# Kernel tuning notes

Hardware: AMD Instinct MI355X
Metric: run time of the kernel (lower is better)

The kernel has to match this reference:

```python
import jax, jax.numpy as jnp
import numpy as np

A = 81          # agents / zones (9x9 grid)
DMAX = 5        # max neighborhood size (self + 4-neighbors)
NGLOB = 48      # global obs block width
HID = 128
B = 16384
LN_EPS = 1e-12  # tf.contrib.layers.layer_norm epsilon
BN_EPS = 1e-3   # tf.contrib.layers.batch_norm epsilon
NEG = -1e30


def _grid_adjacency():
    side = 9
    idx = np.zeros((A, DMAX), np.int32)
    mask = np.zeros((A, DMAX), bool)
    for i in range(A):
        r, c = divmod(i, side)
        nb = [i]
        for dr, dc in ((-1, 0), (1, 0), (0, -1), (0, 1)):
            rr, cc = r + dr, c + dc
            if 0 <= rr < side and 0 <= cc < side:
                nb.append(rr * side + cc)
        idx[i, :len(nb)] = nb
        mask[i, :len(nb)] = True
    return jnp.asarray(idx), jnp.asarray(mask)


def setup_inputs() -> dict:
    key = jax.random.key(0)
    ks = jax.random.split(key, 8)
    neigh_idx, neigh_mask = _grid_adjacency()
    in_dim = 2 * DMAX + NGLOB  # padded local obs width (58)
    s = 0.05
    return {
        "obs": jax.random.normal(ks[0], (B, 210), jnp.float32),
        "neigh_idx": neigh_idx,
        "neigh_mask": neigh_mask,
        "W1": jax.random.normal(ks[1], (A, in_dim, HID), jnp.float32) * s,
        "b1": jnp.zeros((A, HID), jnp.float32),
        "ln1_g": jnp.ones((A, HID), jnp.float32),
        "ln1_b": jnp.zeros((A, HID), jnp.float32),
        "bn1_b": jnp.zeros((A, HID), jnp.float32),
        "W2": jax.random.normal(ks[2], (A, HID, HID), jnp.float32) * s,
        "b2": jnp.zeros((A, HID), jnp.float32),
        "ln2_g": jnp.ones((A, HID), jnp.float32),
        "ln2_b": jnp.zeros((A, HID), jnp.float32),
        "bn2_b": jnp.zeros((A, HID), jnp.float32),
        "Wout": jax.random.normal(ks[3], (A, HID, DMAX), jnp.float32) * s,
        "bout": jnp.zeros((A, DMAX), jnp.float32),
    }


def _layer_norm(x, g, b):
    mu = jnp.mean(x, axis=-1, keepdims=True)
    var = jnp.mean(jnp.square(x - mu), axis=-1, keepdims=True)
    return (x - mu) * jax.lax.rsqrt(var + LN_EPS) * g[:, None, :] + b[:, None, :]


def _batch_norm(x, beta):
    # training-mode batch norm over the batch axis (axis=1), center only (scale=False)
    mu = jnp.mean(x, axis=1, keepdims=True)
    var = jnp.mean(jnp.square(x - mu), axis=1, keepdims=True)
    return (x - mu) * jax.lax.rsqrt(var + BN_EPS) + beta[:, None, :]


def reference(obs, neigh_idx, neigh_mask, W1, b1, ln1_g, ln1_b, bn1_b,
              W2, b2, ln2_g, ln2_b, bn2_b, Wout, bout):
    m = neigh_mask[:, None, :].astype(obs.dtype)          # [A,1,DMAX]
    g1 = obs[:, NGLOB + neigh_idx].transpose(1, 0, 2)      # [A,B,DMAX] zone block 1
    g2 = obs[:, NGLOB + 81 + neigh_idx].transpose(1, 0, 2)  # [A,B,DMAX] zone block 2
    glob = jnp.broadcast_to(obs[None, :, :NGLOB], (A, obs.shape[0], NGLOB))
    x = jnp.concatenate([g1 * m, g2 * m, glob], axis=-1)   # [A,B,58] (padded slots zeroed)

    h = jnp.einsum('abi,aio->abo', x, W1) + b1[:, None, :]
    h = jax.nn.relu(_batch_norm(_layer_norm(h, ln1_g, ln1_b), bn1_b))
    h = jnp.einsum('abi,aio->abo', h, W2) + b2[:, None, :]
    h = jax.nn.relu(_batch_norm(_layer_norm(h, ln2_g, ln2_b), bn2_b))

    logits = jnp.einsum('abi,aid->abd', h, Wout) + bout[:, None, :]  # [A,B,DMAX]
    logits = jnp.where(neigh_mask[:, None, :], logits, NEG)
    p = jax.nn.softmax(logits, axis=-1) * m                # masked softmax over valid neighbors

    oh = jax.nn.one_hot(neigh_idx, A, dtype=p.dtype)       # [A,DMAX,81] scatter map
    out = jnp.einsum('abd,adn->abn', p, oh)                # scatter into fixed 81-vector
    return out.transpose(1, 0, 2)                          # [B,A,81]
```

## Files before the change

### kernel.cpp

```cpp
#include <hip/hip_runtime.h>
#include <stdint.h>
#include <stddef.h>

#define N_AG 81

typedef __bf16 bf16x8 __attribute__((ext_vector_type(8)));
typedef float f32x4 __attribute__((ext_vector_type(4)));
typedef uint32_t u32v4 __attribute__((ext_vector_type(4)));
typedef uint32_t u32v2 __attribute__((ext_vector_type(2)));

#define PB 0
#define PG 128
#define PBT 256

#define SWZ(row, off) ((uint32_t)(off) ^ (((uint32_t)(row) & 7u) << 4))

__device__ __forceinline__ unsigned short b2u(__bf16 h) {
  return __builtin_bit_cast(unsigned short, h);
}

__device__ __forceinline__ f32x4 f4z() { f32x4 v; v[0]=0.f; v[1]=0.f; v[2]=0.f; v[3]=0.f; return v; }

__device__ __forceinline__ bf16x8 ld_frag(const uint8_t* p) {
  u32v4 v = *(const u32v4*)p;
  return __builtin_bit_cast(bf16x8, v);
}

__device__ __forceinline__ f32x4 mfma16(bf16x8 a, bf16x8 b, f32x4 c) {
  return __builtin_amdgcn_mfma_f32_16x16x32_bf16(a, b, c, 0, 0, 0);
}

__device__ __forceinline__ uint8_t* yslot(float* out, int b, int a) {
  size_t base = (size_t)b * 26244 + (size_t)a * 324;
  uint32_t pad = (uint32_t)(64 - (base & 63)) & 63u;
  return (uint8_t*)out + base + pad;
}

__device__ __forceinline__ float wave16_sum(float v) {
  v += __builtin_bit_cast(float, __builtin_amdgcn_update_dpp(0, __builtin_bit_cast(int, v), 0xB1, 0xF, 0xF, true));
  v += __builtin_bit_cast(float, __builtin_amdgcn_update_dpp(0, __builtin_bit_cast(int, v), 0x4E, 0xF, 0xF, true));
  v += __builtin_bit_cast(float, __builtin_amdgcn_update_dpp(0, __builtin_bit_cast(int, v), 0x141, 0xF, 0xF, true));
  v += __builtin_bit_cast(float, __builtin_amdgcn_update_dpp(0, __builtin_bit_cast(int, v), 0x140, 0xF, 0xF, true));
  return v;
}

__device__ __forceinline__ bf16x8 mk_frag(const unsigned short (&us)[8]) {
  u32v4 pk;
  pk[0] = (uint32_t)us[0] | ((uint32_t)us[1] << 16);
  pk[1] = (uint32_t)us[2] | ((uint32_t)us[3] << 16);
  pk[2] = (uint32_t)us[4] | ((uint32_t)us[5] << 16);
  pk[3] = (uint32_t)us[6] | ((uint32_t)us[7] << 16);
  return __builtin_bit_cast(bf16x8, pk);
}

__device__ __forceinline__ bf16x8 bn_frag(u32v4 yv, const f32x4 (&cf)[4]) {
  bf16x8 r;
  #pragma unroll
  for (int j = 0; j < 8; ++j) {
    uint32_t us = (j & 1) ? (yv[j >> 1] >> 16) : (yv[j >> 1] & 0xffffu);
    float f = __builtin_bit_cast(float, us << 16);
    float h = fmaf(f, cf[j >> 1][(j & 1) * 2], cf[j >> 1][(j & 1) * 2 + 1]);
    r[j] = (__bf16)fmaxf(h, 0.f);
  }
  return r;
}

__device__ __forceinline__ void bias_ln(f32x4 (&acc)[8][2], const float* s_par, int g) {
  #pragma unroll
  for (int nf = 0; nf < 2; ++nf) {
    float s = 0.f, qs = 0.f;
    #pragma unroll
    for (int mf = 0; mf < 8; ++mf) {
      #pragma unroll
      for (int rg = 0; rg < 4; ++rg) {
        float tv = acc[mf][nf][rg] + s_par[PB + 16 * mf + 4 * g + rg];
        acc[mf][nf][rg] = tv;
        s += tv;
        qs = fmaf(tv, tv, qs);
      }
    }
    s += __shfl_xor(s, 16);  s += __shfl_xor(s, 32);
    qs += __shfl_xor(qs, 16); qs += __shfl_xor(qs, 32);
    float mu = s * (1.f / 128.f);
    float var = qs * (1.f / 128.f) - mu * mu;
    float rstd = rsqrtf(var + 1e-12f);
    #pragma unroll
    for (int mf = 0; mf < 8; ++mf) {
      #pragma unroll
      for (int rg = 0; rg < 4; ++rg) {
        int o = 16 * mf + 4 * g + rg;
        acc[mf][nf][rg] = (acc[mf][nf][rg] - mu) * rstd * s_par[PG + o] + s_par[PBT + o];
      }
    }
  }
}

__device__ __forceinline__ void stats_lds(const f32x4 (&acc)[8][2],
                                          float (&s_red)[2][4][128],
                                          int wv, int g, int q) {
  #pragma unroll
  for (int mf = 0; mf < 8; ++mf) {
    #pragma unroll
    for (int rg = 0; rg < 4; ++rg) {
      float a0v = acc[mf][0][rg], a1v = acc[mf][1][rg];
      float s = a0v + a1v;
      float qq = fmaf(a0v, a0v, a1v * a1v);
      s = wave16_sum(s);
      qq = wave16_sum(qq);
      if (q == 0) {
        int o = 16 * mf + 4 * g + rg;
        s_red[0][wv][o] += s;
        s_red[1][wv][o] += qq;
      }
    }
  }
}

__device__ __forceinline__ void pack_lds(const f32x4 (&acc)[8][2], uint8_t* s_y,
                                         int wv, int g, int q) {
  #pragma unroll
  for (int nf = 0; nf < 2; ++nf) {
    uint32_t row = 32 * wv + 16 * nf + q;
    #pragma unroll
    for (int mf = 0; mf < 8; ++mf) {
      u32v2 pk;
      pk[0] = (uint32_t)b2u((__bf16)acc[mf][nf][0]) | ((uint32_t)b2u((__bf16)acc[mf][nf][1]) << 16);
      pk[1] = (uint32_t)b2u((__bf16)acc[mf][nf][2]) | ((uint32_t)b2u((__bf16)acc[mf][nf][3]) << 16);
      *(u32v2*)(s_y + row * 256 + SWZ(row, 32 * mf + 8 * g)) = pk;
    }
  }
}

__device__ __forceinline__ void burst_out(const uint8_t* s_y, float* out, int tile, int a, int t) {
  const int row = t >> 1, half = t & 1;
  uint8_t* sp = yslot(out, tile * 128 + row, a) + half * 128;
  #pragma unroll
  for (int j = 0; j < 8; ++j) {
    u32v4 v = *(const u32v4*)(s_y + row * 256 + SWZ(row, half * 128 + 16 * j));
    *(u32v4*)(sp + 16 * j) = v;
  }
}

__device__ __forceinline__ void load_yregs(u32v4 (&yr)[8], const float* out, int tile, int a, int t) {
  const int row = t >> 1, half = t & 1;
  const uint8_t* sp = yslot((float*)out, tile * 128 + row, a) + half * 128;
  #pragma unroll
  for (int j = 0; j < 8; ++j) yr[j] = *(const u32v4*)(sp + 16 * j);
}

__device__ __forceinline__ void write_yregs(uint8_t* s_y, const u32v4 (&yr)[8], int t) {
  const int row = t >> 1, half = t & 1;
  #pragma unroll
  for (int j = 0; j < 8; ++j)
    *(u32v4*)(s_y + row * 256 + SWZ(row, half * 128 + 16 * j)) = yr[j];
}

__global__ void prep_w1(const float* __restrict__ W1, uint8_t* __restrict__ w1img) {
  const int a = blockIdx.x, t = threadIdx.x;
  for (int i = t; i < 128 * 64; i += 256) {
    int o = i & 127, kk = i >> 7;
    float v;
    if (kk < 48)      v = W1[((size_t)a * 58 + (10 + kk)) * 128 + o];
    else if (kk < 58) v = W1[((size_t)a * 58 + (kk - 48)) * 128 + o];
    else              v = 0.f;
    uint32_t cb = 2u * kk;
    uint32_t phys = o * 128 + (((cb & ~15u) ^ (((uint32_t)o & 7u) << 4)) | (cb & 15u));
    *(unsigned short*)(w1img + (size_t)a * 16384 + phys) = b2u((__bf16)v);
  }
}

__global__ void prep_w2wo(const float* __restrict__ W2, const float* __restrict__ Wout,
                          uint8_t* __restrict__ w2img, uint8_t* __restrict__ woimg) {
  const int a = blockIdx.x, t = threadIdx.x;
  for (int i = t; i < 128 * 128; i += 256) {
    int o = i & 127, kk = i >> 7;
    float v = W2[((size_t)a * 128 + kk) * 128 + o];
    uint32_t cb = 2u * kk;
    uint32_t phys = o * 256 + (((cb & ~15u) ^ (((uint32_t)o & 7u) << 4)) | (cb & 15u));
    *(unsigned short*)(w2img + (size_t)a * 32768 + phys) = b2u((__bf16)v);
  }
  for (int i = t; i < 16 * 128; i += 256) {
    int k = i & 127, d = i >> 7;
    float v = (d < 5) ? Wout[((size_t)a * 128 + k) * 5 + d] : 0.f;
    uint32_t cb = 2u * k;
    uint32_t phys = d * 256 + (((cb & ~15u) ^ (((uint32_t)d & 7u) << 4)) | (cb & 15u));
    *(unsigned short*)(woimg + (size_t)a * 4096 + phys) = b2u((__bf16)v);
  }
}

__global__ void prep_obs(const float* __restrict__ obs, uint8_t* __restrict__ globimg) {
  const int row = blockIdx.x * 256 + threadIdx.x;
  if (row >= 16384) return;
  const float* orow = obs + (size_t)row * 210;
  uint8_t* dst = globimg + (size_t)row * 96;
  #pragma unroll
  for (int c = 0; c < 6; ++c) {
    u32v4 pk;
    #pragma unroll
    for (int e = 0; e < 4; ++e) {
      pk[e] = (uint32_t)b2u((__bf16)orow[8 * c + 2 * e]) |
              ((uint32_t)b2u((__bf16)orow[8 * c + 2 * e + 1]) << 16);
    }
    *(u32v4*)(dst + 16 * c) = pk;
  }
}

__global__ void prep_zimgT(const float* __restrict__ obs, unsigned short* __restrict__ zimgT) {
  __shared__ unsigned short lt[128][164];
  const int t = threadIdx.x;
  const int b0 = blockIdx.x * 128;
  for (int i = t; i < 128 * 162; i += 256) {
    int br = i / 162, n = i - 162 * br;
    lt[br][n] = b2u((__bf16)obs[(size_t)(b0 + br) * 210 + 48 + n]);
  }
  __syncthreads();
  for (int i = t; i < 162 * 128; i += 256) {
    int n = i >> 7, br = i & 127;
    zimgT[(size_t)n * 16384 + b0 + br] = lt[br][n];
  }
}

__global__ void reduce_bn(const float* __restrict__ S, const float* __restrict__ Q,
                          const float* __restrict__ beta, float2* __restrict__ bn) {
  const int a = blockIdx.x, k = threadIdx.x;
  float mu = S[a * 128 + k] * (1.f / 16384.f);
  float var = Q[a * 128 + k] * (1.f / 16384.f) - mu * mu;
  float rs = rsqrtf(var + 1e-3f);
  bn[a * 128 + k] = make_float2(rs, beta[a * 128 + k] - mu * rs);
}

__launch_bounds__(256, 2)
__global__ void pass1_kernel(const int* __restrict__ nidx,
                             const float* __restrict__ b1, const float* __restrict__ ln1g,
                             const float* __restrict__ ln1b,
                             const uint8_t* __restrict__ w1img,
                             const uint8_t* __restrict__ globimg,
                             const unsigned short* __restrict__ zimgT,
                             float* __restrict__ statS, float* __restrict__ statQ,
                             float* __restrict__ out) {
  __shared__ __align__(16) uint8_t s_w1[16384];
  __shared__ __align__(16) uint8_t s_y[32768];
  __shared__ float s_par[384];
  __shared__ float s_red[2][4][128];

  const int t = threadIdx.x;
  const int wv = t >> 6, l = t & 63, g = l >> 4, q = l & 15;
  const int a = blockIdx.x >> 5;
  const int sub = blockIdx.x & 31;

  const int r9 = a / 9, c9 = a - 9 * r9;
  const int deg = 1 + (r9 > 0) + (r9 < 8) + (c9 > 0) + (c9 < 8);
  int nid[5];
  #pragma unroll
  for (int d = 0; d < 5; ++d) nid[d] = __builtin_amdgcn_readfirstlane(nidx[a * 5 + d]);

  const uint8_t* w1src = w1img + (size_t)a * 16384;
  #pragma unroll
  for (int i = 0; i < 4; ++i) ((u32v4*)s_w1)[t + 256 * i] = ((const u32v4*)w1src)[t + 256 * i];
  if (t < 128) {
    s_par[PB + t] = b1[a * 128 + t];
    s_par[PG + t] = ln1g[a * 128 + t];
    s_par[PBT + t] = ln1b[a * 128 + t];
  }
  #pragma unroll
  for (int i = 0; i < 4; ++i) ((float*)s_red)[t + 256 * i] = 0.f;
  __syncthreads();

  for (int tt = 0; tt < 4; ++tt) {
    const int tile = sub * 4 + tt;

    bf16x8 bfr[2][2];
    #pragma unroll
    for (int ks = 0; ks < 2; ++ks) {
      #pragma unroll
      for (int nf = 0; nf < 2; ++nf) {
        const int brow = tile * 128 + 32 * wv + 16 * nf + q;
        if (ks == 1 && g >= 2) {
          unsigned short us[8];
          if (g == 2) {
            #pragma unroll
            for (int e = 0; e < 5; ++e)
              us[e] = (e < deg) ? zimgT[(size_t)nid[e] * 16384 + brow] : (unsigned short)0;
            #pragma unroll
            for (int e = 0; e < 3; ++e)
              us[5 + e] = (e < deg) ? zimgT[(size_t)(81 + nid[e]) * 16384 + brow] : (unsigned short)0;
          } else {
            us[0] = (3 < deg) ? zimgT[(size_t)(81 + nid[3]) * 16384 + brow] : (unsigned short)0;
            us[1] = (4 < deg) ? zimgT[(size_t)(81 + nid[4]) * 16384 + brow] : (unsigned short)0;
            #pragma unroll
            for (int e = 2; e < 8; ++e) us[e] = 0;
          }
          bfr[ks][nf] = mk_frag(us);
        } else {
          bfr[ks][nf] = *(const bf16x8*)(globimg + (size_t)brow * 96 + (32 * ks + 8 * g) * 2);
        }
      }
    }

    f32x4 acc[8][2];
    #pragma unroll
    for (int mf = 0; mf < 8; ++mf) { acc[mf][0] = f4z(); acc[mf][1] = f4z(); }
    #pragma unroll
    for (int ks = 0; ks < 2; ++ks) {
      #pragma unroll
      for (int mf = 0; mf < 8; ++mf) {
        uint32_t r = 16 * mf + q;
        uint32_t cb = ((uint32_t)(64 * ks + 16 * g)) ^ ((r & 7u) << 4);
        bf16x8 af = ld_frag(s_w1 + r * 128 + cb);
        acc[mf][0] = mfma16(af, bfr[ks][0], acc[mf][0]);
        acc[mf][1] = mfma16(af, bfr[ks][1], acc[mf][1]);
      }
    }

    bias_ln(acc, s_par, g);
    stats_lds(acc, s_red, wv, g, q);
    pack_lds(acc, s_y, wv, g, q);
    burst_out(s_y, out, tile, a, t);
  }

  __syncthreads();
  if (t < 128) {
    float S = s_red[0][0][t] + s_red[0][1][t] + s_red[0][2][t] + s_red[0][3][t];
    float Q = s_red[1][0][t] + s_red[1][1][t] + s_red[1][2][t] + s_red[1][3][t];
    atomicAdd(statS + a * 128 + t, S);
    atomicAdd(statQ + a * 128 + t, Q);
  }
}

__launch_bounds__(256, 2)
__global__ void pass2_kernel(const float* __restrict__ b2, const float* __restrict__ ln2g,
                             const float* __restrict__ ln2b,
                             const uint8_t* __restrict__ w2img,
                             const float2* __restrict__ bn1,
                             float* __restrict__ statS, float* __restrict__ statQ,
                             float* __restrict__ out) {
  __shared__ __align__(16) uint8_t s_w2[32768];
  __shared__ __align__(16) uint8_t s_y[32768];
  __shared__ float s_par[384];
  __shared__ __align__(16) float2 s_bnc[128];
  __shared__ float s_red[2][4][128];

  const int t = threadIdx.x;
  const int wv = t >> 6, l = t & 63, g = l >> 4, q = l & 15;
  const int a = blockIdx.x >> 5;
  const int sub = blockIdx.x & 31;

  const uint8_t* w2src = w2img + (size_t)a * 32768;
  #pragma unroll
  for (int i = 0; i < 8; ++i) ((u32v4*)s_w2)[t + 256 * i] = ((const u32v4*)w2src)[t + 256 * i];
  if (t < 128) {
    s_par[PB + t] = b2[a * 128 + t];
    s_par[PG + t] = ln2g[a * 128 + t];
    s_par[PBT + t] = ln2b[a * 128 + t];
    s_bnc[t] = bn1[a * 128 + t];
  }
  #pragma unroll
  for (int i = 0; i < 4; ++i) ((float*)s_red)[t + 256 * i] = 0.f;

  u32v4 yreg[8];
  load_yregs(yreg, out, sub * 4, a, t);
  __syncthreads();

  for (int tt = 0; tt < 4; ++tt) {
    const int tile = sub * 4 + tt;

    write_yregs(s_y, yreg, t);
    if (tt < 3) load_yregs(yreg, out, tile + 1, a, t);

    f32x4 acc[8][2];
    #pragma unroll
    for (int mf = 0; mf < 8; ++mf) { acc[mf][0] = f4z(); acc[mf][1] = f4z(); }

    #pragma unroll
    for (int ks2 = 0; ks2 < 4; ++ks2) {
      const int k0 = 32 * ks2 + 8 * g;
      f32x4 cf[4];
      #pragma unroll
      for (int i = 0; i < 4; ++i)
        cf[i] = *(const f32x4*)((const uint8_t*)s_bnc + k0 * 8 + 16 * i);
      bf16x8 bfr[2];
      #pragma unroll
      for (int nf = 0; nf < 2; ++nf) {
        uint32_t row = 32 * wv + 16 * nf + q;
        u32v4 yv = *(const u32v4*)(s_y + row * 256 + SWZ(row, 64 * ks2 + 16 * g));
        bfr[nf] = bn_frag(yv, cf);
      }
      #pragma unroll
      for (int mf = 0; mf < 8; ++mf) {
        uint32_t r = 16 * mf + q;
        uint32_t cb = ((uint32_t)(64 * ks2 + 16 * g)) ^ ((r & 7u) << 4);
        bf16x8 af = ld_frag(s_w2 + r * 256 + cb);
        acc[mf][0] = mfma16(af, bfr[0], acc[mf][0]);
        acc[mf][1] = mfma16(af, bfr[1], acc[mf][1]);
      }
    }

    bias_ln(acc, s_par, g);
    stats_lds(acc, s_red, wv, g, q);
    pack_lds(acc, s_y, wv, g, q);
    burst_out(s_y, out, tile, a, t);
  }

  __syncthreads();
  if (t < 128) {
    float S = s_red[0][0][t] + s_red[0][1][t] + s_red[0][2][t] + s_red[0][3][t];
    float Q = s_red[1][0][t] + s_red[1][1][t] + s_red[1][2][t] + s_red[1][3][t];
    atomicAdd(statS + a * 128 + t, S);
    atomicAdd(statQ + a * 128 + t, Q);
  }
}

__launch_bounds__(256, 3)
__global__ void pass3_kernel(const int* __restrict__ nidx, const float* __restrict__ boutp,
                             const uint8_t* __restrict__ woimg,
                             const float2* __restrict__ bn2,
                             float* __restrict__ out) {
  __shared__ __align__(16) uint8_t s_buf[43008];
  __shared__ __align__(16) uint8_t s_wo[4096];
  __shared__ __align__(16) float2 s_bnc[128];
  __shared__ float s_bout[16];

  uint8_t* s_y = s_buf;
  float* s_out = (float*)s_buf;

  const int t = threadIdx.x;
  const int wv = t >> 6, l = t & 63, g = l >> 4, q = l & 15;
  const int a = blockIdx.x >> 5;
  const int sub = blockIdx.x & 31;

  const int r9 = a / 9, c9 = a - 9 * r9;
  const int deg = 1 + (r9 > 0) + (r9 < 8) + (c9 > 0) + (c9 < 8);
  int nid[5];
  #pragma unroll
  for (int d = 0; d < 5; ++d) nid[d] = __builtin_amdgcn_readfirstlane(nidx[a * 5 + d]);

  ((u32v4*)s_wo)[t] = ((const u32v4*)(woimg + (size_t)a * 4096))[t];
  if (t < 128) s_bnc[t] = bn2[a * 128 + t];
  if (t < 16) s_bout[t] = (t < 5) ? boutp[a * 5 + t] : 0.f;

  u32v4 yreg[8];
  load_yregs(yreg, out, sub * 4, a, t);
  __syncthreads();

  bf16x8 afr[4];
  #pragma unroll
  for (int ks2 = 0; ks2 < 4; ++ks2) {
    uint32_t cb = ((uint32_t)(64 * ks2 + 16 * g)) ^ (((uint32_t)q & 7u) << 4);
    afr[ks2] = ld_frag(s_wo + q * 256 + cb);
  }

  for (int tt = 0; tt < 4; ++tt) {
    const int tile = sub * 4 + tt;

    write_yregs(s_y, yreg, t);
    if (tt < 3) load_yregs(yreg, out, tile + 1, a, t);

    f32x4 accd[2];
    accd[0] = f4z(); accd[1] = f4z();

    #pragma unroll
    for (int ks2 = 0; ks2 < 4; ++ks2) {
      const int k0 = 32 * ks2 + 8 * g;
      f32x4 cf[4];
      #pragma unroll
      for (int i = 0; i < 4; ++i)
        cf[i] = *(const f32x4*)((const uint8_t*)s_bnc + k0 * 8 + 16 * i);
      #pragma unroll
      for (int nf = 0; nf < 2; ++nf) {
        uint32_t row = 32 * wv + 16 * nf + q;
        u32v4 yv = *(const u32v4*)(s_y + row * 256 + SWZ(row, 64 * ks2 + 16 * g));
        accd[nf] = mfma16(afr[ks2], bn_frag(yv, cf), accd[nf]);
      }
    }

    #pragma unroll
    for (int nf = 0; nf < 2; ++nf) {
      #pragma unroll
      for (int rg = 0; rg < 4; ++rg) accd[nf][rg] += s_bout[4 * g + rg];
    }
    float d4[2];
    d4[0] = __shfl_xor(accd[0][0], 16);
    d4[1] = __shfl_xor(accd[1][0], 16);

    float p[2][5];
    #pragma unroll
    for (int nf = 0; nf < 2; ++nf) {
      float v[5] = {accd[nf][0], accd[nf][1], accd[nf][2], accd[nf][3], d4[nf]};
      float mx = v[0];
      #pragma unroll
      for (int d = 1; d < 5; ++d)
        if (d < deg) mx = fmaxf(mx, v[d]);
      float den = 0.f;
      #pragma unroll
      for (int d = 0; d < 5; ++d) {
        float e = (d < deg) ? __expf(v[d] - mx) : 0.f;
        p[nf][d] = e;
        den += e;
      }
      float inv = 1.f / den;
      #pragma unroll
      for (int d = 0; d < 5; ++d) p[nf][d] *= inv;
    }

    float p5[5];
    #pragma unroll
    for (int d = 0; d < 5; ++d) {
      float pr = __shfl_xor(p[1][d], 32);
      p5[d] = (g == 0) ? p[0][d] : pr;
    }

    __syncthreads();

    {
      const uint32_t fbase = 84u * 32u * wv;
      for (int i = l; i < 672; i += 64) {
        u32v4 z; z[0] = 0u; z[1] = 0u; z[2] = 0u; z[3] = 0u;
        *(u32v4*)((uint8_t*)s_out + (size_t)fbase * 4 + (size_t)i * 16) = z;
      }
      if (g == 0 || g == 2) {
        const int row = 32 * wv + ((g == 2) ? 16 : 0) + q;
        #pragma unroll
        for (int d = 0; d < 5; ++d)
          if (d < deg) s_out[row * 84 + nid[d]] = p5[d];
      }
      const size_t obase = (size_t)(tile * 128) * 6561 + (size_t)a * 81;
      for (int i = l; i < 32 * 81; i += 64) {
        int rr = i / 81;
        int n = i - rr * 81;
        int row = 32 * wv + rr;
        out[obase + (size_t)row * 6561 + n] = s_out[row * 84 + n];
      }
    }

    __syncthreads();
  }
}

extern "C" void kernel_launch(void* const* d_in, const int* in_sizes, int n_in,
                              void* d_out, int out_size, void* d_ws, size_t ws_size,
                              hipStream_t stream) {
  (void)in_sizes; (void)n_in; (void)out_size; (void)ws_size;
  const float* obs = (const float*)d_in[0];
  const int* nidx = (const int*)d_in[1];
  const float* W1 = (const float*)d_in[3];
  const float* b1 = (const float*)d_in[4];
  const float* ln1g = (const float*)d_in[5];
  const float* ln1b = (const float*)d_in[6];
  const float* bnb1 = (const float*)d_in[7];
  const float* W2 = (const float*)d_in[8];
  const float* b2 = (const float*)d_in[9];
  const float* ln2g = (const float*)d_in[10];
  const float* ln2b = (const float*)d_in[11];
  const float* bnb2 = (const float*)d_in[12];
  const float* Wout = (const float*)d_in[13];
  const float* bout = (const float*)d_in[14];
  float* out = (float*)d_out;
  uint8_t* ws = (uint8_t*)d_ws;

  uint8_t* w1img   = ws;
  uint8_t* globimg = ws + 1327104;
  uint8_t* regionA = ws + 2899968;
  unsigned short* zimgT = (unsigned short*)regionA;
  uint8_t* w2img = regionA;
  uint8_t* woimg = regionA + 2654208;
  float* statS = (float*)(ws + 8208384);
  float* statQ = (float*)(ws + 8249856);
  float2* bn1 = (float2*)(ws + 8291328);
  float2* bn2 = (float2*)(ws + 8374272);

  prep_w1<<<N_AG, 256, 0, stream>>>(W1, w1img);
  prep_obs<<<64, 256, 0, stream>>>(obs, globimg);
  prep_zimgT<<<128, 256, 0, stream>>>(obs, zimgT);
  hipMemsetAsync(statS, 0, 2 * 41472, stream);

  pass1_kernel<<<N_AG * 32, 256, 0, stream>>>(nidx, b1, ln1g, ln1b, w1img, globimg, zimgT,
                                              statS, statQ, out);
  reduce_bn<<<N_AG, 128, 0, stream>>>(statS, statQ, bnb1, bn1);

  prep_w2wo<<<N_AG, 256, 0, stream>>>(W2, Wout, w2img, woimg);
  hipMemsetAsync(statS, 0, 2 * 41472, stream);

  pass2_kernel<<<N_AG * 32, 256, 0, stream>>>(b2, ln2g, ln2b, w2img, bn1,
                                              statS, statQ, out);
  reduce_bn<<<N_AG, 128, 0, stream>>>(statS, statQ, bnb2, bn2);

  pass3_kernel<<<N_AG * 32, 256, 0, stream>>>(nidx, bout, woimg, bn2, out);
}
```

Baseline: 934.9 us.

## Shrink pass1 tiles, raise occupancy, remap block-to-agent order, fold stat memsets

Pass1 now handles 64-row sub-tiles with a single N-fragment, so its accumulator register footprint and LDS staging buffer are halved, and launch bounds rise to 4 blocks per CU. Block IDs in all three passes are remapped so that consecutive blocks cover different agents, spreading work and memory traffic. The two statistic memsets are removed: prep_w1 zeroes the buffers first and reduce_bn re-zeroes them after reading. The price is more loop iterations and barriers per block in pass1, and possible register spills under the tighter launch bound.

Measured after the change: 754.4 us. -19.3%, faster.

```diff
diff --git a/kernel.cpp b/kernel.cpp
--- a/kernel.cpp
+++ b/kernel.cpp
@@ -28,6 +28,12 @@
 
 __device__ __forceinline__ f32x4 mfma16(bf16x8 a, bf16x8 b, f32x4 c) {
   return __builtin_amdgcn_mfma_f32_16x16x32_bf16(a, b, c, 0, 0, 0);
+}
+
+__device__ __forceinline__ void work_id(int bid, int& a, int& sub) {
+  int w = (bid & 7) * 324 + (bid >> 3);
+  a = w % N_AG;
+  sub = w / N_AG;
 }
 
 __device__ __forceinline__ uint8_t* yslot(float* out, int b, int a) {
@@ -91,6 +97,33 @@
         int o = 16 * mf + 4 * g + rg;
         acc[mf][nf][rg] = (acc[mf][nf][rg] - mu) * rstd * s_par[PG + o] + s_par[PBT + o];
       }
+    }
+  }
+}
+
+__device__ __forceinline__ void bias_ln1(f32x4 (&acc)[8], const float* s_par, int g) {
+  float s = 0.f, qs = 0.f;
+  #pragma unroll
+  for (int mf = 0; mf < 8; ++mf) {
+    #pragma unroll
+    for (int rg = 0; rg < 4; ++rg) {
+      float tv = acc[mf][rg] + s_par[PB + 16 * mf + 4 * g + rg];
+      acc[mf][rg] = tv;
+      s += tv;
+      qs = fmaf(tv, tv, qs);
+    }
+  }
+  s += __shfl_xor(s, 16);  s += __shfl_xor(s, 32);
+  qs += __shfl_xor(qs, 16); qs += __shfl_xor(qs, 32);
+  float mu = s * (1.f / 128.f);
+  float var = qs * (1.f / 128.f) - mu * mu;
+  float rstd = rsqrtf(var + 1e-12f);
+  #pragma unroll
+  for (int mf = 0; mf < 8; ++mf) {
+    #pragma unroll
+    for (int rg = 0; rg < 4; ++rg) {
+      int o = 16 * mf + 4 * g + rg;
+      acc[mf][rg] = (acc[mf][rg] - mu) * rstd * s_par[PG + o] + s_par[PBT + o];
     }
   }
 }
@@ -116,6 +149,26 @@
   }
 }
 
+__device__ __forceinline__ void stats_lds1(const f32x4 (&acc)[8],
+                                           float (&s_red)[2][4][128],
+                                           int wv, int g, int q) {
+  #pragma unroll
+  for (int mf = 0; mf < 8; ++mf) {
+    #pragma unroll
+    for (int rg = 0; rg < 4; ++rg) {
+      float s = acc[mf][rg];
+      float qq = s * s;
+      s = wave16_sum(s);
+      qq = wave16_sum(qq);
+      if (q == 0) {
+        int o = 16 * mf + 4 * g + rg;
+        s_red[0][wv][o] += s;
+        s_red[1][wv][o] += qq;
+      }
+    }
+  }
+}
+
 __device__ __forceinline__ void pack_lds(const f32x4 (&acc)[8][2], uint8_t* s_y,
                                          int wv, int g, int q) {
   #pragma unroll
@@ -131,6 +184,18 @@
   }
 }
 
+__device__ __forceinline__ void pack_lds1(const f32x4 (&acc)[8], uint8_t* s_y,
+                                          int wv, int g, int q) {
+  uint32_t row = 16 * wv + q;
+  #pragma unroll
+  for (int mf = 0; mf < 8; ++mf) {
+    u32v2 pk;
+    pk[0] = (uint32_t)b2u((__bf16)acc[mf][0]) | ((uint32_t)b2u((__bf16)acc[mf][1]) << 16);
+    pk[1] = (uint32_t)b2u((__bf16)acc[mf][2]) | ((uint32_t)b2u((__bf16)acc[mf][3]) << 16);
+    *(u32v2*)(s_y + row * 256 + SWZ(row, 32 * mf + 8 * g)) = pk;
+  }
+}
+
 __device__ __forceinline__ void burst_out(const uint8_t* s_y, float* out, int tile, int a, int t) {
   const int row = t >> 1, half = t & 1;
   uint8_t* sp = yslot(out, tile * 128 + row, a) + half * 128;
@@ -141,6 +206,16 @@
   }
 }
 
+__device__ __forceinline__ void burst_out64(const uint8_t* s_y, float* out, int base, int a, int t) {
+  const int row = t >> 2, qt = t & 3;
+  uint8_t* sp = yslot(out, base + row, a) + qt * 64;
+  #pragma unroll
+  for (int j = 0; j < 4; ++j) {
+    u32v4 v = *(const u32v4*)(s_y + row * 256 + SWZ(row, qt * 64 + 16 * j));
+    *(u32v4*)(sp + 16 * j) = v;
+  }
+}
+
 __device__ __forceinline__ void load_yregs(u32v4 (&yr)[8], const float* out, int tile, int a, int t) {
   const int row = t >> 1, half = t & 1;
   const uint8_t* sp = yslot((float*)out, tile * 128 + row, a) + half * 128;
@@ -155,7 +230,8 @@
     *(u32v4*)(s_y + row * 256 + SWZ(row, half * 128 + 16 * j)) = yr[j];
 }
 
-__global__ void prep_w1(const float* __restrict__ W1, uint8_t* __restrict__ w1img) {
+__global__ void prep_w1(const float* __restrict__ W1, uint8_t* __restrict__ w1img,
+                        float* __restrict__ statS, float* __restrict__ statQ) {
   const int a = blockIdx.x, t = threadIdx.x;
   for (int i = t; i < 128 * 64; i += 256) {
     int o = i & 127, kk = i >> 7;
@@ -167,6 +243,10 @@
     uint32_t phys = o * 128 + (((cb & ~15u) ^ (((uint32_t)o & 7u) << 4)) | (cb & 15u));
     *(unsigned short*)(w1img + (size_t)a * 16384 + phys) = b2u((__bf16)v);
   }
+  if (t < 128) {
+    statS[a * 128 + t] = 0.f;
+    statQ[a * 128 + t] = 0.f;
+  }
 }
 
 __global__ void prep_w2wo(const float* __restrict__ W2, const float* __restrict__ Wout,
@@ -220,16 +300,18 @@
   }
 }
 
-__global__ void reduce_bn(const float* __restrict__ S, const float* __restrict__ Q,
+__global__ void reduce_bn(float* __restrict__ S, float* __restrict__ Q,
                           const float* __restrict__ beta, float2* __restrict__ bn) {
   const int a = blockIdx.x, k = threadIdx.x;
   float mu = S[a * 128 + k] * (1.f / 16384.f);
   float var = Q[a * 128 + k] * (1.f / 16384.f) - mu * mu;
   float rs = rsqrtf(var + 1e-3f);
   bn[a * 128 + k] = make_float2(rs, beta[a * 128 + k] - mu * rs);
-}
-
-__launch_bounds__(256, 2)
+  S[a * 128 + k] = 0.f;
+  Q[a * 128 + k] = 0.f;
+}
+
+__launch_bounds__(256, 4)
 __global__ void pass1_kernel(const int* __restrict__ nidx,
                              const float* __restrict__ b1, const float* __restrict__ ln1g,
                              const float* __restrict__ ln1b,
@@ -239,14 +321,14 @@
                              float* __restrict__ statS, float* __restrict__ statQ,
                              float* __restrict__ out) {
   __shared__ __align__(16) uint8_t s_w1[16384];
-  __shared__ __align__(16) uint8_t s_y[32768];
+  __shared__ __align__(16) uint8_t s_y[16384];
   __shared__ float s_par[384];
   __shared__ float s_red[2][4][128];
 
   const int t = threadIdx.x;
   const int wv = t >> 6, l = t & 63, g = l >> 4, q = l & 15;
-  const int a = blockIdx.x >> 5;
-  const int sub = blockIdx.x & 31;
+  int a, sub;
+  work_id(blockIdx.x, a, sub);
 
   const int r9 = a / 9, c9 = a - 9 * r9;
   const int deg = 1 + (r9 > 0) + (r9 < 8) + (c9 > 0) + (c9 < 8);
@@ -266,40 +348,37 @@
   for (int i = 0; i < 4; ++i) ((float*)s_red)[t + 256 * i] = 0.f;
   __syncthreads();
 
-  for (int tt = 0; tt < 4; ++tt) {
-    const int tile = sub * 4 + tt;
-
-    bf16x8 bfr[2][2];
+  for (int hh = 0; hh < 8; ++hh) {
+    const int base = sub * 512 + hh * 64;
+    const int brow = base + 16 * wv + q;
+
+    bf16x8 bfr[2];
     #pragma unroll
     for (int ks = 0; ks < 2; ++ks) {
-      #pragma unroll
-      for (int nf = 0; nf < 2; ++nf) {
-        const int brow = tile * 128 + 32 * wv + 16 * nf + q;
-        if (ks == 1 && g >= 2) {
-          unsigned short us[8];
-          if (g == 2) {
-            #pragma unroll
-            for (int e = 0; e < 5; ++e)
-              us[e] = (e < deg) ? zimgT[(size_t)nid[e] * 16384 + brow] : (unsigned short)0;
-            #pragma unroll
-            for (int e = 0; e < 3; ++e)
-              us[5 + e] = (e < deg) ? zimgT[(size_t)(81 + nid[e]) * 16384 + brow] : (unsigned short)0;
-          } else {
-            us[0] = (3 < deg) ? zimgT[(size_t)(81 + nid[3]) * 16384 + brow] : (unsigned short)0;
-            us[1] = (4 < deg) ? zimgT[(size_t)(81 + nid[4]) * 16384 + brow] : (unsigned short)0;
-            #pragma unroll
-            for (int e = 2; e < 8; ++e) us[e] = 0;
-          }
-          bfr[ks][nf] = mk_frag(us);
+      if (ks == 1 && g >= 2) {
+        unsigned short us[8];
+        if (g == 2) {
+          #pragma unroll
+          for (int e = 0; e < 5; ++e)
+            us[e] = (e < deg) ? zimgT[(size_t)nid[e] * 16384 + brow] : (unsigned short)0;
+          #pragma unroll
+          for (int e = 0; e < 3; ++e)
+            us[5 + e] = (e < deg) ? zimgT[(size_t)(81 + nid[e]) * 16384 + brow] : (unsigned short)0;
         } else {
-          bfr[ks][nf] = *(const bf16x8*)(globimg + (size_t)brow * 96 + (32 * ks + 8 * g) * 2);
+          us[0] = (3 < deg) ? zimgT[(size_t)(81 + nid[3]) * 16384 + brow] : (unsigned short)0;
+          us[1] = (4 < deg) ? zimgT[(size_t)(81 + nid[4]) * 16384 + brow] : (unsigned short)0;
+          #pragma unroll
+          for (int e = 2; e < 8; ++e) us[e] = 0;
         }
-      }
-    }
-
-    f32x4 acc[8][2];
-    #pragma unroll
-    for (int mf = 0; mf < 8; ++mf) { acc[mf][0] = f4z(); acc[mf][1] = f4z(); }
+        bfr[ks] = mk_frag(us);
+      } else {
+        bfr[ks] = *(const bf16x8*)(globimg + (size_t)brow * 96 + (32 * ks + 8 * g) * 2);
+      }
+    }
+
+    f32x4 acc[8];
+    #pragma unroll
+    for (int mf = 0; mf < 8; ++mf) acc[mf] = f4z();
     #pragma unroll
     for (int ks = 0; ks < 2; ++ks) {
       #pragma unroll
@@ -307,18 +386,17 @@
         uint32_t r = 16 * mf + q;
         uint32_t cb = ((uint32_t)(64 * ks + 16 * g)) ^ ((r & 7u) << 4);
         bf16x8 af = ld_frag(s_w1 + r * 128 + cb);
-        acc[mf][0] = mfma16(af, bfr[ks][0], acc[mf][0]);
-        acc[mf][1] = mfma16(af, bfr[ks][1], acc[mf][1]);
-      }
-    }
-
-    bias_ln(acc, s_par, g);
-    stats_lds(acc, s_red, wv, g, q);
-    pack_lds(acc, s_y, wv, g, q);
-    burst_out(s_y, out, tile, a, t);
-  }
-
-  __syncthreads();
+        acc[mf] = mfma16(af, bfr[ks], acc[mf]);
+      }
+    }
+
+    bias_ln1(acc, s_par, g);
+    stats_lds1(acc, s_red, wv, g, q);
+    pack_lds1(acc, s_y, wv, g, q);
+    burst_out64(s_y, out, base, a, t);
+    __syncthreads();
+  }
+
   if (t < 128) {
     float S = s_red[0][0][t] + s_red[0][1][t] + s_red[0][2][t] + s_red[0][3][t];
     float Q = s_red[1][0][t] + s_red[1][1][t] + s_red[1][2][t] + s_red[1][3][t];
@@ -342,8 +420,8 @@
 
   const int t = threadIdx.x;
   const int wv = t >> 6, l = t & 63, g = l >> 4, q = l & 15;
-  const int a = blockIdx.x >> 5;
-  const int sub = blockIdx.x & 31;
+  int a, sub;
+  work_id(blockIdx.x, a, sub);
 
   const uint8_t* w2src = w2img + (size_t)a * 32768;
   #pragma unroll
@@ -399,9 +477,9 @@
     stats_lds(acc, s_red, wv, g, q);
     pack_lds(acc, s_y, wv, g, q);
     burst_out(s_y, out, tile, a, t);
-  }
-
-  __syncthreads();
+    __syncthreads();
+  }
+
   if (t < 128) {
     float S = s_red[0][0][t] + s_red[0][1][t] + s_red[0][2][t] + s_red[0][3][t];
     float Q = s_red[1][0][t] + s_red[1][1][t] + s_red[1][2][t] + s_red[1][3][t];
@@ -425,8 +503,8 @@
 
   const int t = threadIdx.x;
   const int wv = t >> 6, l = t & 63, g = l >> 4, q = l & 15;
-  const int a = blockIdx.x >> 5;
-  const int sub = blockIdx.x & 31;
+  int a, sub;
+  work_id(blockIdx.x, a, sub);
 
   const int r9 = a / 9, c9 = a - 9 * r9;
   const int deg = 1 + (r9 > 0) + (r9 < 8) + (c9 > 0) + (c9 < 8);
@@ -512,10 +590,10 @@
     __syncthreads();
 
     {
-      const uint32_t fbase = 84u * 32u * wv;
+      uint8_t* band = (uint8_t*)s_out + (size_t)wv * 10752;
       for (int i = l; i < 672; i += 64) {
         u32v4 z; z[0] = 0u; z[1] = 0u; z[2] = 0u; z[3] = 0u;
-        *(u32v4*)((uint8_t*)s_out + (size_t)fbase * 4 + (size_t)i * 16) = z;
+        *(u32v4*)(band + (size_t)i * 16) = z;
       }
       if (g == 0 || g == 2) {
         const int row = 32 * wv + ((g == 2) ? 16 : 0) + q;
@@ -568,17 +646,15 @@
   float2* bn1 = (float2*)(ws + 8291328);
   float2* bn2 = (float2*)(ws + 8374272);
 
-  prep_w1<<<N_AG, 256, 0, stream>>>(W1, w1img);
+  prep_w1<<<N_AG, 256, 0, stream>>>(W1, w1img, statS, statQ);
   prep_obs<<<64, 256, 0, stream>>>(obs, globimg);
   prep_zimgT<<<128, 256, 0, stream>>>(obs, zimgT);
-  hipMemsetAsync(statS, 0, 2 * 41472, stream);
 
   pass1_kernel<<<N_AG * 32, 256, 0, stream>>>(nidx, b1, ln1g, ln1b, w1img, globimg, zimgT,
                                               statS, statQ, out);
   reduce_bn<<<N_AG, 128, 0, stream>>>(statS, statQ, bnb1, bn1);
 
   prep_w2wo<<<N_AG, 256, 0, stream>>>(W2, Wout, w2img, woimg);
-  hipMemsetAsync(statS, 0, 2 * 41472, stream);
 
   pass2_kernel<<<N_AG * 32, 256, 0, stream>>>(b2, ln2g, ln2b, w2img, bn1,
                                               statS, statQ, out);
```
